# Kernel optimization log

Hardware: AMD Instinct MI355X
Metric: run time of the kernel (lower is better)

Reference implementation:

```python
import jax, jax.numpy as jnp
import numpy as np

NUM_USERS = 50000
NUM_ITEMS = 50000
NUM_NODES = NUM_USERS + NUM_ITEMS
EMB_DIM = 128
NUM_LAYERS = 3
NUM_EDGES = 2000000
AVG_DEG = NUM_EDGES / NUM_NODES  # ~20, used to normalize edge weights


def setup_inputs() -> dict:
    key = jax.random.key(0)
    k1, k2, k3, k4 = jax.random.split(key, 4)
    # Xavier-uniform-ish embedding init
    emb_weight = jax.random.normal(k1, (NUM_NODES, EMB_DIM), dtype=jnp.float32) * (1.0 / np.sqrt(EMB_DIM))
    rows = jax.random.randint(k2, (NUM_EDGES,), 0, NUM_NODES, dtype=jnp.int32)
    cols = jax.random.randint(k3, (NUM_EDGES,), 0, NUM_NODES, dtype=jnp.int32)
    # positive normalized edge weights, ~1/deg so spectral radius stays ~1
    vals = jax.random.uniform(k4, (NUM_EDGES,), dtype=jnp.float32) * jnp.float32(2.0 / AVG_DEG)
    return {"emb_weight": emb_weight, "rows": rows, "cols": cols, "vals": vals}


def reference(emb_weight, rows, cols, vals):
    # LightGCN.get_user_item_emb(): multi-layer SpMM propagation + layer mean.
    N = emb_weight.shape[0]

    def spmm(x):
        # out[r] += vals[e] * x[cols[e]] for each edge e with rows[e] == r
        return jax.ops.segment_sum(vals[:, None] * x[cols], rows, num_segments=N)

    x = emb_weight
    acc = x  # running sum of layer outputs (fused stack+mean)
    for _ in range(NUM_LAYERS):
        x = spmm(x)
        acc = acc + x
    x_final = acc / jnp.float32(NUM_LAYERS + 1)
    user_emb = x_final[:NUM_USERS]
    item_emb = x_final[NUM_USERS:]
    return user_emb, item_emb
```

## Files before the change

kernel.cpp:

```cpp
#include <hip/hip_runtime.h>
#include <hip/hip_fp16.h>


#define DIM 128
#define PB   256
#define KPAD 512
#define RPB  256

static inline size_t align_up(size_t v, size_t a) { return (v + a - 1) & ~(a - 1); }

__global__ void lgcn_conv(const float2* __restrict__ emb, __half2* __restrict__ x0,
                          int n2) {
    int i = blockIdx.x * blockDim.x + threadIdx.x;
    if (i < n2) x0[i] = __float22half2_rn(emb[i]);
}

__global__ void __launch_bounds__(256)
lgcn_phist(const int* __restrict__ rows, int* __restrict__ ghist, int nedges) {
    __shared__ int h[KPAD];
    const int b = blockIdx.x, tid = threadIdx.x;
    for (int k = tid; k < KPAD; k += 256) h[k] = 0;
    __syncthreads();
    const int chunk = (nedges + PB - 1) / PB;
    const int beg = b * chunk;
    const int end = min(beg + chunk, nedges);
    for (int e = beg + tid; e < end; e += 256)
        atomicAdd(&h[rows[e] >> 8], 1);
    __syncthreads();
    for (int k = tid; k < KPAD; k += 256) ghist[(k << 8) + b] = h[k];
}

__global__ void __launch_bounds__(256)
lgcn_scan1(const int* __restrict__ counts, int* __restrict__ outp,
           int* __restrict__ bsums, int n) {
    __shared__ int wsum[4];
    const int tid  = threadIdx.x;
    const int lane = tid & 63;
    const int wid  = tid >> 6;
    const int i0   = blockIdx.x * 1024 + tid * 4;

    int c0 = 0, c1 = 0, c2 = 0, c3 = 0;
    if (i0 + 3 < n) {
        int4 c = *(const int4*)(counts + i0);
        c0 = c.x; c1 = c.y; c2 = c.z; c3 = c.w;
    } else {
        if (i0 + 0 < n) c0 = counts[i0 + 0];
        if (i0 + 1 < n) c1 = counts[i0 + 1];
        if (i0 + 2 < n) c2 = counts[i0 + 2];
        if (i0 + 3 < n) c3 = counts[i0 + 3];
    }
    const int t1 = c0 + c1, t2 = t1 + c2, tsum = t2 + c3;

    int incl = tsum;
    #pragma unroll
    for (int off = 1; off < 64; off <<= 1) {
        int t = __shfl_up(incl, off, 64);
        if (lane >= off) incl += t;
    }
    if (lane == 63) wsum[wid] = incl;
    __syncthreads();
    int woff = 0;
    #pragma unroll
    for (int w = 0; w < 4; ++w) woff += (w < wid) ? wsum[w] : 0;

    const int ex = woff + incl - tsum;
    if (i0 + 0 < n) outp[i0 + 0] = ex;
    if (i0 + 1 < n) outp[i0 + 1] = ex + c0;
    if (i0 + 2 < n) outp[i0 + 2] = ex + t1;
    if (i0 + 3 < n) outp[i0 + 3] = ex + t2;
    if (tid == 255) bsums[blockIdx.x] = woff + incl;
}

__global__ void __launch_bounds__(128)
lgcn_scan2(int* __restrict__ bsums, int* __restrict__ outp, int nb, int n) {
    __shared__ int w0s;
    const int tid  = threadIdx.x;
    const int lane = tid & 63;
    const int wid  = tid >> 6;
    int v = (tid < nb) ? bsums[tid] : 0;
    int incl = v;
    #pragma unroll
    for (int off = 1; off < 64; off <<= 1) {
        int t = __shfl_up(incl, off, 64);
        if (lane >= off) incl += t;
    }
    if (tid == 63) w0s = incl;
    __syncthreads();
    const int ex = incl - v + ((wid == 1) ? w0s : 0);
    if (tid < nb) bsums[tid] = ex;
    if (tid == nb - 1) outp[n] = ex + v;
}

__global__ void lgcn_scan3(int* __restrict__ outp, const int* __restrict__ bsums,
                           int n) {
    int i = blockIdx.x * blockDim.x + threadIdx.x;
    if (i < n) outp[i] += bsums[i >> 10];
}

__global__ void __launch_bounds__(256)
lgcn_part(const int* __restrict__ rows, const int* __restrict__ cols,
          const float* __restrict__ vals, const int* __restrict__ gbase,
          int2* __restrict__ staging, int nedges) {
    __shared__ int lcnt[KPAD];
    const int b = blockIdx.x, tid = threadIdx.x;
    for (int k = tid; k < KPAD; k += 256) lcnt[k] = gbase[(k << 8) + b];
    __syncthreads();
    const int chunk = (nedges + PB - 1) / PB;
    const int beg = b * chunk;
    const int end = min(beg + chunk, nedges);
    for (int e = beg + tid; e < end; e += 256) {
        int r   = rows[e];
        int pos = atomicAdd(&lcnt[r >> 8], 1);
        staging[pos] = make_int2(cols[e] | ((r & 255) << 17), __float_as_int(vals[e]));
    }
}

__global__ void __launch_bounds__(256)
lgcn_place(const int* __restrict__ gbase, const int2* __restrict__ staging,
           int* __restrict__ row_ptr, int2* __restrict__ edges, int n, int nbuck) {
    __shared__ int rcnt[RPB];
    __shared__ int cur[RPB];
    __shared__ int wsum[4];
    const int k    = blockIdx.x;
    const int tid  = threadIdx.x;
    const int lane = tid & 63;
    const int wid  = tid >> 6;
    const int base = gbase[k << 8];
    const int next = gbase[(k + 1) << 8];

    rcnt[tid] = 0;
    __syncthreads();
    for (int i = base + tid; i < next; i += 256)
        atomicAdd(&rcnt[(staging[i].x >> 17) & 255], 1);
    __syncthreads();

    const int v = rcnt[tid];
    int incl = v;
    #pragma unroll
    for (int off = 1; off < 64; off <<= 1) {
        int t = __shfl_up(incl, off, 64);
        if (lane >= off) incl += t;
    }
    if (lane == 63) wsum[wid] = incl;
    __syncthreads();
    int woff = 0;
    #pragma unroll
    for (int w = 0; w < 4; ++w) woff += (w < wid) ? wsum[w] : 0;
    const int ex = woff + incl - v;

    cur[tid] = base + ex;
    const int r = (k << 8) + tid;
    if (r < n) row_ptr[r] = base + ex;
    if (k == nbuck - 1 && tid == 0) row_ptr[n] = next;
    __syncthreads();

    for (int i = base + tid; i < next; i += 256) {
        int2 p  = staging[i];
        int pos = atomicAdd(&cur[(p.x >> 17) & 255], 1);
        edges[pos] = make_int2(p.x & 0x1FFFF, p.y);
    }
}

__global__ void __launch_bounds__(256)
lgcn_spmm(const int* __restrict__ row_ptr, const int2* __restrict__ edges,
          const __half2* __restrict__ xin, __half2* __restrict__ xout,
          const float2* __restrict__ emb, const __half2* __restrict__ x1h,
          float2* __restrict__ out, int n, int mode) {
    const int wave = blockIdx.x * 4 + (threadIdx.x >> 6);
    const int lane = threadIdx.x & 63;
    const int g    = lane >> 4;
    const int l    = lane & 15;
    if (wave >= n) return;
    const int beg = row_ptr[wave];
    const int end = row_ptr[wave + 1];

    const int4* __restrict__ x4 = (const int4*)xin;

    float a0 = 0.f, a1 = 0.f, a2 = 0.f, a3 = 0.f;
    float a4 = 0.f, a5 = 0.f, a6 = 0.f, a7 = 0.f;

#define FMA8(Q, V)                                                        \
    {                                                                     \
        float2 f0 = __half22float2(*(const __half2*)&(Q).x);              \
        float2 f1 = __half22float2(*(const __half2*)&(Q).y);              \
        float2 f2 = __half22float2(*(const __half2*)&(Q).z);              \
        float2 f3 = __half22float2(*(const __half2*)&(Q).w);              \
        a0 = fmaf((V), f0.x, a0); a1 = fmaf((V), f0.y, a1);               \
        a2 = fmaf((V), f1.x, a2); a3 = fmaf((V), f1.y, a3);               \
        a4 = fmaf((V), f2.x, a4); a5 = fmaf((V), f2.y, a5);               \
        a6 = fmaf((V), f3.x, a6); a7 = fmaf((V), f3.y, a7);               \
    }

    int e = beg;
    for (; e + 16 <= end; e += 16) {
        int2 d0 = edges[e + g];
        int2 d1 = edges[e + 4 + g];
        int2 d2 = edges[e + 8 + g];
        int2 d3 = edges[e + 12 + g];
        int4 q0 = x4[d0.x * 16 + l];
        int4 q1 = x4[d1.x * 16 + l];
        int4 q2 = x4[d2.x * 16 + l];
        int4 q3 = x4[d3.x * 16 + l];
        FMA8(q0, __int_as_float(d0.y));
        FMA8(q1, __int_as_float(d1.y));
        FMA8(q2, __int_as_float(d2.y));
        FMA8(q3, __int_as_float(d3.y));
    }
    for (; e + 8 <= end; e += 8) {
        int2 d0 = edges[e + g];
        int2 d1 = edges[e + 4 + g];
        int4 q0 = x4[d0.x * 16 + l];
        int4 q1 = x4[d1.x * 16 + l];
        FMA8(q0, __int_as_float(d0.y));
        FMA8(q1, __int_as_float(d1.y));
    }
    for (; e < end; e += 4) {
        const int ee = e + g;
        int2 d = (ee < end) ? edges[ee] : make_int2(0, 0);
        int4 q = x4[d.x * 16 + l];
        FMA8(q, __int_as_float(d.y));
    }
#undef FMA8

    a0 += __shfl_xor(a0, 16); a0 += __shfl_xor(a0, 32);
    a1 += __shfl_xor(a1, 16); a1 += __shfl_xor(a1, 32);
    a2 += __shfl_xor(a2, 16); a2 += __shfl_xor(a2, 32);
    a3 += __shfl_xor(a3, 16); a3 += __shfl_xor(a3, 32);
    a4 += __shfl_xor(a4, 16); a4 += __shfl_xor(a4, 32);
    a5 += __shfl_xor(a5, 16); a5 += __shfl_xor(a5, 32);
    a6 += __shfl_xor(a6, 16); a6 += __shfl_xor(a6, 32);
    a7 += __shfl_xor(a7, 16); a7 += __shfl_xor(a7, 32);

    if (mode == 0) {
        if (g == 0) {
            int4 r;
            __half2 h0 = __float22half2_rn(make_float2(a0, a1));
            __half2 h1 = __float22half2_rn(make_float2(a2, a3));
            __half2 h2 = __float22half2_rn(make_float2(a4, a5));
            __half2 h3 = __float22half2_rn(make_float2(a6, a7));
            r.x = *(const int*)&h0; r.y = *(const int*)&h1;
            r.z = *(const int*)&h2; r.w = *(const int*)&h3;
            ((int4*)xout)[wave * 16 + l] = r;
        }
    } else {
        float4 e0 = ((const float4*)emb)[wave * 32 + l * 2 + 0];
        float4 e1 = ((const float4*)emb)[wave * 32 + l * 2 + 1];
        int4  h1q = ((const int4*)x1h)[wave * 16 + l];
        int4  h2q = ((const int4*)xin)[wave * 16 + l];
        float2 b0 = __half22float2(*(const __half2*)&h1q.x);
        float2 b1 = __half22float2(*(const __half2*)&h1q.y);
        float2 b2 = __half22float2(*(const __half2*)&h1q.z);
        float2 b3 = __half22float2(*(const __half2*)&h1q.w);
        float2 c0 = __half22float2(*(const __half2*)&h2q.x);
        float2 c1 = __half22float2(*(const __half2*)&h2q.y);
        float2 c2 = __half22float2(*(const __half2*)&h2q.z);
        float2 c3 = __half22float2(*(const __half2*)&h2q.w);
        if (g == 0) {
            float4 r0, r1;
            r0.x = (e0.x + b0.x + c0.x + a0) * 0.25f;
            r0.y = (e0.y + b0.y + c0.y + a1) * 0.25f;
            r0.z = (e0.z + b1.x + c1.x + a2) * 0.25f;
            r0.w = (e0.w + b1.y + c1.y + a3) * 0.25f;
            r1.x = (e1.x + b2.x + c2.x + a4) * 0.25f;
            r1.y = (e1.y + b2.y + c2.y + a5) * 0.25f;
            r1.z = (e1.z + b3.x + c3.x + a6) * 0.25f;
            r1.w = (e1.w + b3.y + c3.y + a7) * 0.25f;
            ((float4*)out)[wave * 32 + l * 2 + 0] = r0;
            ((float4*)out)[wave * 32 + l * 2 + 1] = r1;
        }
    }
}

extern "C" void kernel_launch(void* const* d_in, const int* in_sizes, int n_in,
                              void* d_out, int out_size, void* d_ws, size_t ws_size,
                              hipStream_t stream) {
    const float* emb  = (const float*)d_in[0];
    const int*   rows = (const int*)d_in[1];
    const int*   cols = (const int*)d_in[2];
    const float* vals = (const float*)d_in[3];

    const int  n_nodes = in_sizes[0] / DIM;
    const int  nedges  = in_sizes[1];
    const long nd      = (long)n_nodes * DIM;

    char* ws = (char*)d_ws;
    size_t off = 0;
    __half2* bufA = (__half2*)(ws + off); off = align_up(off + nd * 2, 256);
    __half2* bufB = (__half2*)(ws + off); off = align_up(off + nd * 2, 256);
    int2* edges   = (int2*)(ws + off);    off = align_up(off + (size_t)nedges * 8, 256);
    int* row_ptr  = (int*)(ws + off);     off = align_up(off + (size_t)(n_nodes + 1) * 4, 256);
    int* ghist    = (int*)(ws + off);     off = align_up(off + (size_t)KPAD * PB * 4, 256);
    int* gbase    = (int*)(ws + off);     off = align_up(off + ((size_t)KPAD * PB + 1) * 4, 256);
    int* bsums    = (int*)(ws + off);     off = align_up(off + 1024, 256);
    float2* out   = (float2*)d_out;

    int2* staging = (int2*)bufB;

    const int BS = 256;
    const int n2      = (int)(nd / 2);
    const int grid_c  = (n2 + BS - 1) / BS;
    const int nbuck   = (n_nodes + RPB - 1) / RPB;
    const int nscan   = KPAD * PB;
    const int nb      = nscan / 1024;
    const int grid_s  = (n_nodes + 3) / 4;

    lgcn_conv<<<grid_c, BS, 0, stream>>>((const float2*)emb, bufA, n2);

    lgcn_phist<<<PB, BS, 0, stream>>>(rows, ghist, nedges);
    lgcn_scan1<<<nb, BS, 0, stream>>>(ghist, gbase, bsums, nscan);
    lgcn_scan2<<<1, 128, 0, stream>>>(bsums, gbase, nb, nscan);
    lgcn_scan3<<<nscan / BS, BS, 0, stream>>>(gbase, bsums, nscan);
    lgcn_part<<<PB, BS, 0, stream>>>(rows, cols, vals, gbase, staging, nedges);
    lgcn_place<<<nbuck, BS, 0, stream>>>(gbase, staging, row_ptr, edges, n_nodes, nbuck);

    lgcn_spmm<<<grid_s, BS, 0, stream>>>(row_ptr, edges, bufA, bufB,
                                         nullptr, nullptr, nullptr, n_nodes, 0);
    lgcn_spmm<<<grid_s, BS, 0, stream>>>(row_ptr, edges, bufB, bufA,
                                         nullptr, nullptr, nullptr, n_nodes, 0);
    lgcn_spmm<<<grid_s, BS, 0, stream>>>(row_ptr, edges, bufA, nullptr,
                                         (const float2*)emb, bufB, out, n_nodes, 1);
}
```

Before: 418.2 us.

## Fuse preprocessing launches, use decoupled-lookback single-pass scan, cache buckets in LDS

Merges the fp16 conversion and the row histogram into one launch that also zeroes the scan tile-status array. The three-kernel scan becomes a single-pass scan in which each tile looks back at earlier tiles' published status flags. The place kernel keeps each bucket's staging entries in shared memory, so it reads staging from global memory once instead of twice. These changes cut launch count and global traffic in the CSR build, at the cost of spin-waiting between scan tiles and a large LDS allocation (about 57KB) that may lower occupancy in the place kernel.

```diff
diff --git a/kernel.cpp b/kernel.cpp
--- a/kernel.cpp
+++ b/kernel.cpp
@@ -2,54 +2,53 @@
 #include <hip/hip_fp16.h>
 
 
-#define DIM 128
+#define DIM  128
 #define PB   256
 #define KPAD 512
 #define RPB  256
+#define NSCAN (KPAD * PB)
+#define NTILES (NSCAN / 1024)
+#define PCAP 7168
 
 static inline size_t align_up(size_t v, size_t a) { return (v + a - 1) & ~(a - 1); }
 
-__global__ void lgcn_conv(const float2* __restrict__ emb, __half2* __restrict__ x0,
-                          int n2) {
-    int i = blockIdx.x * blockDim.x + threadIdx.x;
-    if (i < n2) x0[i] = __float22half2_rn(emb[i]);
-}
-
-__global__ void __launch_bounds__(256)
-lgcn_phist(const int* __restrict__ rows, int* __restrict__ ghist, int nedges) {
+__global__ void __launch_bounds__(256)
+lgcn_prep(const float2* __restrict__ emb, __half2* __restrict__ x0, int n2,
+          const int* __restrict__ rows, int* __restrict__ ghist, int nedges,
+          unsigned long long* __restrict__ tstat) {
     __shared__ int h[KPAD];
     const int b = blockIdx.x, tid = threadIdx.x;
-    for (int k = tid; k < KPAD; k += 256) h[k] = 0;
-    __syncthreads();
-    const int chunk = (nedges + PB - 1) / PB;
-    const int beg = b * chunk;
-    const int end = min(beg + chunk, nedges);
-    for (int e = beg + tid; e < end; e += 256)
-        atomicAdd(&h[rows[e] >> 8], 1);
-    __syncthreads();
-    for (int k = tid; k < KPAD; k += 256) ghist[(k << 8) + b] = h[k];
-}
-
-__global__ void __launch_bounds__(256)
-lgcn_scan1(const int* __restrict__ counts, int* __restrict__ outp,
-           int* __restrict__ bsums, int n) {
+    if (b < PB) {
+        for (int k = tid; k < KPAD; k += 256) h[k] = 0;
+        __syncthreads();
+        const int chunk = (nedges + PB - 1) / PB;
+        const int beg = b * chunk;
+        const int end = min(beg + chunk, nedges);
+        for (int e = beg + tid; e < end; e += 256)
+            atomicAdd(&h[rows[e] >> 8], 1);
+        __syncthreads();
+        for (int k = tid; k < KPAD; k += 256) ghist[(k << 8) + b] = h[k];
+    } else if (b == PB) {
+        if (tid < NTILES) tstat[tid] = 0ull;
+    } else {
+        const int i = (b - PB - 1) * 256 + tid;
+        if (i < n2) x0[i] = __float22half2_rn(emb[i]);
+    }
+}
+
+__global__ void __launch_bounds__(256)
+lgcn_scan(const int* __restrict__ ghist, int* __restrict__ gbase,
+          unsigned long long* __restrict__ tstat, int nscan) {
     __shared__ int wsum[4];
+    __shared__ int btot_s, prev_s;
+    const int tile = blockIdx.x;
     const int tid  = threadIdx.x;
     const int lane = tid & 63;
     const int wid  = tid >> 6;
-    const int i0   = blockIdx.x * 1024 + tid * 4;
-
-    int c0 = 0, c1 = 0, c2 = 0, c3 = 0;
-    if (i0 + 3 < n) {
-        int4 c = *(const int4*)(counts + i0);
-        c0 = c.x; c1 = c.y; c2 = c.z; c3 = c.w;
-    } else {
-        if (i0 + 0 < n) c0 = counts[i0 + 0];
-        if (i0 + 1 < n) c1 = counts[i0 + 1];
-        if (i0 + 2 < n) c2 = counts[i0 + 2];
-        if (i0 + 3 < n) c3 = counts[i0 + 3];
-    }
-    const int t1 = c0 + c1, t2 = t1 + c2, tsum = t2 + c3;
+    const int i0   = tile * 1024 + tid * 4;
+
+    int4 c = *(const int4*)(ghist + i0);
+    const int t1 = c.x + c.y, t2 = t1 + c.z, tsum = t2 + c.w;
 
     int incl = tsum;
     #pragma unroll
@@ -62,39 +61,47 @@
     int woff = 0;
     #pragma unroll
     for (int w = 0; w < 4; ++w) woff += (w < wid) ? wsum[w] : 0;
-
     const int ex = woff + incl - tsum;
-    if (i0 + 0 < n) outp[i0 + 0] = ex;
-    if (i0 + 1 < n) outp[i0 + 1] = ex + c0;
-    if (i0 + 2 < n) outp[i0 + 2] = ex + t1;
-    if (i0 + 3 < n) outp[i0 + 3] = ex + t2;
-    if (tid == 255) bsums[blockIdx.x] = woff + incl;
-}
-
-__global__ void __launch_bounds__(128)
-lgcn_scan2(int* __restrict__ bsums, int* __restrict__ outp, int nb, int n) {
-    __shared__ int w0s;
-    const int tid  = threadIdx.x;
-    const int lane = tid & 63;
-    const int wid  = tid >> 6;
-    int v = (tid < nb) ? bsums[tid] : 0;
-    int incl = v;
-    #pragma unroll
-    for (int off = 1; off < 64; off <<= 1) {
-        int t = __shfl_up(incl, off, 64);
-        if (lane >= off) incl += t;
-    }
-    if (tid == 63) w0s = incl;
-    __syncthreads();
-    const int ex = incl - v + ((wid == 1) ? w0s : 0);
-    if (tid < nb) bsums[tid] = ex;
-    if (tid == nb - 1) outp[n] = ex + v;
-}
-
-__global__ void lgcn_scan3(int* __restrict__ outp, const int* __restrict__ bsums,
-                           int n) {
-    int i = blockIdx.x * blockDim.x + threadIdx.x;
-    if (i < n) outp[i] += bsums[i >> 10];
+    if (tid == 255) btot_s = woff + incl;
+    __syncthreads();
+    const int btot = btot_s;
+
+    if (tid == 0) {
+        if (tile == 0) {
+            __hip_atomic_store(&tstat[0],
+                (((unsigned long long)(unsigned)btot) << 32) | 2ull,
+                __ATOMIC_RELEASE, __HIP_MEMORY_SCOPE_AGENT);
+            prev_s = 0;
+        } else {
+            __hip_atomic_store(&tstat[tile],
+                (((unsigned long long)(unsigned)btot) << 32) | 1ull,
+                __ATOMIC_RELEASE, __HIP_MEMORY_SCOPE_AGENT);
+            int t = tile - 1, run = 0;
+            while (true) {
+                unsigned long long st = __hip_atomic_load(&tstat[t],
+                    __ATOMIC_ACQUIRE, __HIP_MEMORY_SCOPE_AGENT);
+                unsigned f = (unsigned)st & 3u;
+                if (f == 0u) { __builtin_amdgcn_s_sleep(1); continue; }
+                run += (int)(unsigned)(st >> 32);
+                if (f == 2u) break;
+                --t;
+            }
+            __hip_atomic_store(&tstat[tile],
+                (((unsigned long long)(unsigned)(run + btot)) << 32) | 2ull,
+                __ATOMIC_RELEASE, __HIP_MEMORY_SCOPE_AGENT);
+            prev_s = run;
+        }
+    }
+    __syncthreads();
+    const int pv = prev_s;
+
+    int4 o;
+    o.x = pv + ex;
+    o.y = pv + ex + c.x;
+    o.z = pv + ex + t1;
+    o.w = pv + ex + t2;
+    *(int4*)(gbase + i0) = o;
+    if (tile == gridDim.x - 1 && tid == 255) gbase[nscan] = pv + btot;
 }
 
 __global__ void __launch_bounds__(256)
@@ -121,17 +128,28 @@
     __shared__ int rcnt[RPB];
     __shared__ int cur[RPB];
     __shared__ int wsum[4];
+    __shared__ int2 cache[PCAP];
     const int k    = blockIdx.x;
     const int tid  = threadIdx.x;
     const int lane = tid & 63;
     const int wid  = tid >> 6;
     const int base = gbase[k << 8];
     const int next = gbase[(k + 1) << 8];
+    const int cnt  = next - base;
+    const bool fit = (cnt <= PCAP);
 
     rcnt[tid] = 0;
     __syncthreads();
-    for (int i = base + tid; i < next; i += 256)
-        atomicAdd(&rcnt[(staging[i].x >> 17) & 255], 1);
+    if (fit) {
+        for (int i = tid; i < cnt; i += 256) {
+            int2 p = staging[base + i];
+            cache[i] = p;
+            atomicAdd(&rcnt[(p.x >> 17) & 255], 1);
+        }
+    } else {
+        for (int i = base + tid; i < next; i += 256)
+            atomicAdd(&rcnt[(staging[i].x >> 17) & 255], 1);
+    }
     __syncthreads();
 
     const int v = rcnt[tid];
@@ -154,10 +172,18 @@
     if (k == nbuck - 1 && tid == 0) row_ptr[n] = next;
     __syncthreads();
 
-    for (int i = base + tid; i < next; i += 256) {
-        int2 p  = staging[i];
-        int pos = atomicAdd(&cur[(p.x >> 17) & 255], 1);
-        edges[pos] = make_int2(p.x & 0x1FFFF, p.y);
+    if (fit) {
+        for (int i = tid; i < cnt; i += 256) {
+            int2 p  = cache[i];
+            int pos = atomicAdd(&cur[(p.x >> 17) & 255], 1);
+            edges[pos] = make_int2(p.x & 0x1FFFF, p.y);
+        }
+    } else {
+        for (int i = base + tid; i < next; i += 256) {
+            int2 p  = staging[i];
+            int pos = atomicAdd(&cur[(p.x >> 17) & 255], 1);
+            edges[pos] = make_int2(p.x & 0x1FFFF, p.y);
+        }
     }
 }
 
@@ -289,9 +315,10 @@
     __half2* bufB = (__half2*)(ws + off); off = align_up(off + nd * 2, 256);
     int2* edges   = (int2*)(ws + off);    off = align_up(off + (size_t)nedges * 8, 256);
     int* row_ptr  = (int*)(ws + off);     off = align_up(off + (size_t)(n_nodes + 1) * 4, 256);
-    int* ghist    = (int*)(ws + off);     off = align_up(off + (size_t)KPAD * PB * 4, 256);
-    int* gbase    = (int*)(ws + off);     off = align_up(off + ((size_t)KPAD * PB + 1) * 4, 256);
-    int* bsums    = (int*)(ws + off);     off = align_up(off + 1024, 256);
+    int* ghist    = (int*)(ws + off);     off = align_up(off + (size_t)NSCAN * 4, 256);
+    int* gbase    = (int*)(ws + off);     off = align_up(off + ((size_t)NSCAN + 1) * 4, 256);
+    unsigned long long* tstat = (unsigned long long*)(ws + off);
+    off = align_up(off + (size_t)NTILES * 8, 256);
     float2* out   = (float2*)d_out;
 
     int2* staging = (int2*)bufB;
@@ -300,16 +327,11 @@
     const int n2      = (int)(nd / 2);
     const int grid_c  = (n2 + BS - 1) / BS;
     const int nbuck   = (n_nodes + RPB - 1) / RPB;
-    const int nscan   = KPAD * PB;
-    const int nb      = nscan / 1024;
     const int grid_s  = (n_nodes + 3) / 4;
 
-    lgcn_conv<<<grid_c, BS, 0, stream>>>((const float2*)emb, bufA, n2);
-
-    lgcn_phist<<<PB, BS, 0, stream>>>(rows, ghist, nedges);
-    lgcn_scan1<<<nb, BS, 0, stream>>>(ghist, gbase, bsums, nscan);
-    lgcn_scan2<<<1, 128, 0, stream>>>(bsums, gbase, nb, nscan);
-    lgcn_scan3<<<nscan / BS, BS, 0, stream>>>(gbase, bsums, nscan);
+    lgcn_prep<<<PB + 1 + grid_c, BS, 0, stream>>>((const float2*)emb, bufA, n2,
+                                                  rows, ghist, nedges, tstat);
+    lgcn_scan<<<NTILES, BS, 0, stream>>>(ghist, gbase, tstat, NSCAN);
     lgcn_part<<<PB, BS, 0, stream>>>(rows, cols, vals, gbase, staging, nedges);
     lgcn_place<<<nbuck, BS, 0, stream>>>(gbase, staging, row_ptr, edges, n_nodes, nbuck);
 
```

Result: no change. 420.0 us (+0.4%).
